# Optimization experiments

Measured on AMD Instinct MI355X. Metric: run time of the kernel, lower is better.

The kernel has to match this reference:

```python
import jax, jax.numpy as jnp
import numpy as np

BS, SEQ, E, H, NG, NH = 512, 32, 1024, 1024, 3, 2
MID = SEQ - NG + 1  # 30 (fusion_bidir is Linear(60, 30) -> 2*MID == 60)


def setup_inputs() -> dict:
    key = jax.random.key(0)
    ks = jax.random.split(key, 15)
    sE, sH, sNH = E ** -0.5, H ** -0.5, NH ** -0.5
    f32 = jnp.float32
    return {
        "x": jax.random.normal(ks[0], (BS, SEQ, E), f32),
        "h0": jax.random.normal(ks[1], (2, BS, H), f32),
        "Wz": jax.random.normal(ks[2], (2, H, E), f32) * sE,
        "Uz": jax.random.normal(ks[3], (2, H, H), f32) * sH,
        "Wr": jax.random.normal(ks[4], (2, H, E), f32) * sE,
        "Ur": jax.random.normal(ks[5], (2, H, H), f32) * sH,
        "Wh": jax.random.normal(ks[6], (2, H, E), f32) * sE,
        "Uh": jax.random.normal(ks[7], (2, H, H), f32) * sH,
        "Ua": jax.random.normal(ks[8], (2, NH, E), f32) * sE,      # Ua1: Linear(E,1) per head
        "Wa_w": jax.random.normal(ks[9], (2, NH, NG, H), f32) * sH, # Wa1: Linear(H,NG) per head
        "Wa_b": jax.random.normal(ks[10], (2, NH, NG), f32) * sH,
        "fh_w": jax.random.normal(ks[11], (2, NH), f32) * sNH,      # fusion_head: Linear(NH,1)
        "fh_b": jax.random.normal(ks[12], (2,), f32) * sNH,
        "fb_w": jax.random.normal(ks[13], (30, 60), f32) * (60 ** -0.5),
        "fb_b": jax.random.normal(ks[14], (30,), f32) * (60 ** -0.5),
    }


def _forward_dir(x, h0, Wz, Uz, Wr, Ur, Wh, Uh, Ua, Wa_w, Wa_b, fh_w, fh_b):
    # x: [bs, SEQ, E]; h0: [bs, H]; returns [bs, MID, E]
    idx = jnp.arange(MID)[:, None] + jnp.arange(NG)[None, :]   # [MID, NG]
    xw = x[:, idx, :]                                          # [bs, MID, NG, E] windows
    ua = jnp.einsum('bmge,he->bmgh', xw, Ua)                   # Ua1(x_) per head
    xs = xw.sum(2)                                             # [bs, MID, E] window sum
    # precompute input projections of GRU gates (big GEMMs, hoisted out of scan)
    pz = jnp.einsum('bme,de->bmd', xs, Wz)
    pr = jnp.einsum('bme,de->bmd', xs, Wr)
    ph = jnp.einsum('bme,de->bmd', xs, Wh)
    seqs = (ua.transpose(1, 0, 2, 3), xw.transpose(1, 0, 2, 3),
            pz.transpose(1, 0, 2), pr.transpose(1, 0, 2), ph.transpose(1, 0, 2))

    def step(ht, s):
        ua_t, xw_t, pz_t, pr_t, ph_t = s
        # attention scores: Ua1(x_) + Wa1(ht), fused over heads, tanh, softmax over window
        wa = jnp.einsum('bd,hgd->bgh', ht, Wa_w) + Wa_b.T[None]    # [bs, NG, NH]
        et = jnp.tanh(jnp.einsum('bgh,h->bg', ua_t + wa, fh_w) + fh_b)
        alpha = jax.nn.softmax(et, axis=1)                          # [bs, NG]
        out = jnp.einsum('bge,bg->be', xw_t, alpha)                 # weighted window sum
        # GRU gates on the (unweighted) window sum, as in the original
        zt = jax.nn.sigmoid(pz_t + ht @ Uz.T)
        rt = jax.nn.sigmoid(pr_t + ht @ Ur.T)
        hw = jnp.tanh(ph_t + (rt * ht) @ Uh.T)
        ht_new = (1.0 - zt) * ht + zt * hw
        return ht_new, out

    _, outs = jax.lax.scan(step, h0, seqs)       # outs: [MID, bs, E]
    return outs.transpose(1, 0, 2)


def reference(x, h0, Wz, Uz, Wr, Ur, Wh, Uh, Ua, Wa_w, Wa_b, fh_w, fh_b, fb_w, fb_b):
    X0 = _forward_dir(x, h0[0], Wz[0], Uz[0], Wr[0], Ur[0], Wh[0], Uh[0],
                      Ua[0], Wa_w[0], Wa_b[0], fh_w[0], fh_b[0])
    X1 = _forward_dir(x[:, ::-1, :], h0[1], Wz[1], Uz[1], Wr[1], Ur[1], Wh[1], Uh[1],
                      Ua[1], Wa_w[1], Wa_b[1], fh_w[1], fh_b[1])
    Xb = jnp.concatenate([X0, X1], axis=1).transpose(0, 2, 1)   # [bs, E, 2*MID]
    return (Xb @ fb_w.T + fb_b).transpose(0, 2, 1)              # [bs, 30, E]
```

## Files before the change

kernel.cpp:

```cpp
#include <hip/hip_runtime.h>
#include <hip/hip_bf16.h>
#include <math.h>

#define BSZ 512
#define SEQL 32
#define EDIM 1024
#define HDIM 1024
#define MIDL 30

typedef unsigned short u16;
typedef __attribute__((ext_vector_type(8))) short bf16x8_t;
typedef __attribute__((ext_vector_type(4))) float floatx4_t;

__device__ inline u16 f2bf(float v) {
    unsigned u = __float_as_uint(v);
    unsigned r = u + 0x7FFFu + ((u >> 16) & 1u);
    return (u16)(r >> 16);
}
__device__ inline float bf2f(u16 h) { return __uint_as_float(((unsigned)h) << 16); }
__device__ inline void split2(float v, u16& hi, u16& lo) {
    u16 h = f2bf(v);
    hi = h;
    lo = f2bf(v - bf2f(h));
}

#define SWZ(r, cb) (((r) << 7) + ((cb) ^ (((r) & 7) << 4)))

#define GLOAD16(g, l)                                                    \
    __builtin_amdgcn_global_load_lds(                                    \
        (const __attribute__((address_space(1))) void*)(g),              \
        (__attribute__((address_space(3))) void*)(l), 16, 0, 0)

__global__ __launch_bounds__(256) void convert_w(const float* __restrict__ src,
                                                 u16* __restrict__ hi,
                                                 u16* __restrict__ lo,
                                                 int writeLo) {
    size_t i = ((size_t)blockIdx.x * 256 + threadIdx.x) * 4;
    float4 v = *(const float4*)(src + i);
    u16 hx, lx, hy, ly, hz, lz, hw, lw;
    split2(v.x, hx, lx); split2(v.y, hy, ly);
    split2(v.z, hz, lz); split2(v.w, hw, lw);
    ushort4 hv; hv.x = hx; hv.y = hy; hv.z = hz; hv.w = hw;
    *(ushort4*)(hi + i) = hv;
    if (writeLo) {
        ushort4 lv; lv.x = lx; lv.y = ly; lv.z = lz; lv.w = lw;
        *(ushort4*)(lo + i) = lv;
    }
}

__global__ __launch_bounds__(256) void init_h(const float* __restrict__ h0,
                                              float* __restrict__ hbuf,
                                              u16* __restrict__ hhi,
                                              u16* __restrict__ hlo) {
    size_t i = ((size_t)blockIdx.x * 256 + threadIdx.x) * 4;
    float4 v = *(const float4*)(h0 + i);
    *(float4*)(hbuf + i) = v;
    u16 hx, lx, hy, ly, hz, lz, hw, lw;
    split2(v.x, hx, lx); split2(v.y, hy, ly);
    split2(v.z, hz, lz); split2(v.w, hw, lw);
    ushort4 hv; hv.x = hx; hv.y = hy; hv.z = hz; hv.w = hw;
    ushort4 lv; lv.x = lx; lv.y = ly; lv.z = lz; lv.w = lw;
    *(ushort4*)(hhi + i) = hv;
    *(ushort4*)(hlo + i) = lv;
}

__global__ __launch_bounds__(256) void xs_build(const float* __restrict__ x,
                                                u16* __restrict__ xshi,
                                                u16* __restrict__ xslo,
                                                int writeLo) {
    int idx = blockIdx.x * 256 + threadIdx.x;
    int vid = idx & 255;
    int bw = idx >> 8;
    int w = bw % 30, b = bw / 30;
    const float* s = x + ((size_t)b * SEQL + w) * EDIM + vid * 4;
    float4 a = *(const float4*)s;
    float4 c = *(const float4*)(s + EDIM);
    float4 e = *(const float4*)(s + 2 * EDIM);
    float4 v; v.x = a.x + c.x + e.x; v.y = a.y + c.y + e.y;
    v.z = a.z + c.z + e.z; v.w = a.w + c.w + e.w;
    size_t o = ((size_t)b * 30 + w) * EDIM + vid * 4;
    u16 hx, lx, hy, ly, hz, lz, hw, lw;
    split2(v.x, hx, lx); split2(v.y, hy, ly);
    split2(v.z, hz, lz); split2(v.w, hw, lw);
    ushort4 hv; hv.x = hx; hv.y = hy; hv.z = hz; hv.w = hw;
    *(ushort4*)(xshi + o) = hv;
    if (writeLo) {
        ushort4 lv; lv.x = lx; lv.y = ly; lv.z = lz; lv.w = lw;
        *(ushort4*)(xslo + o) = lv;
    }
}

__global__ __launch_bounds__(256) void ua2_kernel(const float* __restrict__ x,
                                                  const float* __restrict__ Ua,
                                                  float* __restrict__ ua2) {
    int bs = blockIdx.x;
    int b = bs >> 5, s = bs & 31;
    const float* xr = x + ((size_t)b * SEQL + s) * EDIM;
    int tid = threadIdx.x;
    float a[4] = {0.f, 0.f, 0.f, 0.f};
    for (int e = tid; e < EDIM; e += 256) {
        float xv = xr[e];
#pragma unroll
        for (int q = 0; q < 4; q++) a[q] += xv * Ua[q * EDIM + e];
    }
#pragma unroll
    for (int q = 0; q < 4; q++)
        for (int off = 32; off > 0; off >>= 1) a[q] += __shfl_down(a[q], off);
    __shared__ float sr[4][4];
    int wid = tid >> 6, lane = tid & 63;
    if (lane == 0) {
#pragma unroll
        for (int q = 0; q < 4; q++) sr[wid][q] = a[q];
    }
    __syncthreads();
    if (tid < 4) {
        float v = sr[0][tid] + sr[1][tid] + sr[2][tid] + sr[3][tid];
        int d = tid >> 1, h2 = tid & 1;
        ua2[(((size_t)d * BSZ + b) * SEQL + s) * 2 + h2] = v;
    }
}

template<int BM, int MODE, typename XT>
__global__ __launch_bounds__(256) void gemm_step(
    const u16* __restrict__ whi, const u16* __restrict__ wlo,
    const u16* __restrict__ ahi, const u16* __restrict__ alo,
    const u16* __restrict__ xshi, const u16* __restrict__ xslo,
    float* __restrict__ hbuf, float* __restrict__ zbuf,
    u16* __restrict__ ohi, u16* __restrict__ olo,
    const float* __restrict__ x, const float* __restrict__ ua2,
    const float* __restrict__ Wa_w, const float* __restrict__ Wa_b,
    const float* __restrict__ fh_w, const float* __restrict__ fh_b,
    XT* __restrict__ Xbuf,
    int m, int useXsLo, int useWLo) {

    constexpr int MF = BM / 32;
    constexpr int GX = 512 / BM;

    __shared__ __align__(16) u16 AsHi[BM * 64], AsLo[BM * 64];
    __shared__ __align__(16) u16 BsHi[64 * 64], BsLo[64 * 64];
    __shared__ float sred[4][6];

    const int d = blockIdx.z;
    const int tid = threadIdx.x;
    const int wid = tid >> 6, lane = tid & 63;

    if (MODE == 0 && blockIdx.y >= 32) {
        const int b = blockIdx.x * 64 + (blockIdx.y - 32);
        const float* hb = hbuf + ((size_t)d * BSZ + b) * HDIM;
        const float* Ww = Wa_w + (size_t)d * 6 * HDIM;
        float w6[6] = {0.f, 0.f, 0.f, 0.f, 0.f, 0.f};
        for (int j = tid; j < HDIM; j += 256) {
            float hv = hb[j];
#pragma unroll
            for (int q = 0; q < 6; q++) w6[q] += hv * Ww[q * HDIM + j];
        }
#pragma unroll
        for (int q = 0; q < 6; q++)
            for (int off = 32; off > 0; off >>= 1) w6[q] += __shfl_down(w6[q], off);
        if (lane == 0) {
#pragma unroll
            for (int q = 0; q < 6; q++) sred[wid][q] = w6[q];
        }
        __syncthreads();
        float s6[6];
#pragma unroll
        for (int q = 0; q < 6; q++)
            s6[q] = sred[0][q] + sred[1][q] + sred[2][q] + sred[3][q];

        int p0 = (d == 0) ? m : (31 - m);
        int p1 = (d == 0) ? (m + 1) : (30 - m);
        int p2 = (d == 0) ? (m + 2) : (29 - m);
        const float fw0 = fh_w[d * 2 + 0], fw1 = fh_w[d * 2 + 1], fbv = fh_b[d];
        float et[3];
        int pg[3] = {p0, p1, p2};
#pragma unroll
        for (int g = 0; g < 3; g++) {
            const float* u = ua2 + (((size_t)d * BSZ + b) * SEQL + pg[g]) * 2;
            float a0 = u[0] + s6[g] + Wa_b[d * 6 + g];
            float a1 = u[1] + s6[3 + g] + Wa_b[d * 6 + 3 + g];
            et[g] = tanhf(a0 * fw0 + a1 * fw1 + fbv);
        }
        float mx = fmaxf(et[0], fmaxf(et[1], et[2]));
        float e0 = expf(et[0] - mx), e1 = expf(et[1] - mx), e2 = expf(et[2] - mx);
        float inv = 1.f / (e0 + e1 + e2);
        float al0 = e0 * inv, al1 = e1 * inv, al2 = e2 * inv;

        const float* xb = x + (size_t)b * SEQL * EDIM;
        int e4 = tid * 4;
        float4 x0 = *(const float4*)(xb + (size_t)p0 * EDIM + e4);
        float4 x1 = *(const float4*)(xb + (size_t)p1 * EDIM + e4);
        float4 x2 = *(const float4*)(xb + (size_t)p2 * EDIM + e4);
        float4 v; v.x = al0 * x0.x + al1 * x1.x + al2 * x2.x;
        v.y = al0 * x0.y + al1 * x1.y + al2 * x2.y;
        v.z = al0 * x0.z + al1 * x1.z + al2 * x2.z;
        v.w = al0 * x0.w + al1 * x1.w + al2 * x2.w;
        XT* Xo = Xbuf + (((size_t)d * BSZ + b) * MIDL + m) * EDIM + e4;
        if constexpr (sizeof(XT) == 4) {
            *(float4*)Xo = v;
        } else {
            ushort4 uv; uv.x = f2bf(v.x); uv.y = f2bf(v.y);
            uv.z = f2bf(v.z); uv.w = f2bf(v.w);
            *(ushort4*)Xo = uv;
        }
        return;
    }

    const int lin = blockIdx.x + GX * blockIdx.y;
    const int work = (lin & 7) * 32 + (lin >> 3);
    const int b0 = (work & (GX - 1)) * BM;
    const int n0 = (work / GX) * 64;
    const int w = (d == 0) ? m : (29 - m);

    int rgate, nrow0, matU, matW;
    if (MODE == 0) {
        rgate = (n0 >= 1024) ? 1 : 0;
        nrow0 = n0 & 1023;
        matU = rgate ? 1 : 0;
        matW = rgate ? 4 : 3;
    } else {
        rgate = 0; nrow0 = n0; matU = 2; matW = 5;
    }

    floatx4_t acc[MF][2];
#pragma unroll
    for (int i = 0; i < MF; i++)
#pragma unroll
        for (int j = 0; j < 2; j++) acc[i][j] = (floatx4_t){0.f, 0.f, 0.f, 0.f};

    const int wm = wid >> 1, wn = wid & 1;
    const int rr = lane >> 3;
    const int swb = (((lane & 7) ^ rr) << 4);
    const int cA0 = wid, cA1 = wid + 4;
    const int cB0 = wid, cB1 = wid + 4;

    for (int half = 0; half < 2; half++) {
        const size_t wOff = (size_t)(half ? matW : matU) * 2097152 + (size_t)d * 1048576;
        const char* bH = (const char*)(whi + wOff);
        const char* bL = (const char*)(wlo + wOff);
        const int bLoOn = useWLo;
        int aLoOn;
        const char *pa0h, *pa0l, *pa1h = nullptr, *pa1l = nullptr;
        if (half == 0) {
            aLoOn = 1;
            size_t r0 = (size_t)(d * BSZ + b0 + cA0 * 8 + rr) * 2048;
            pa0h = (const char*)ahi + r0 + swb;
            pa0l = (const char*)alo + r0 + swb;
            if (BM == 64) {
                size_t r1 = (size_t)(d * BSZ + b0 + cA1 * 8 + rr) * 2048;
                pa1h = (const char*)ahi + r1 + swb;
                pa1l = (const char*)alo + r1 + swb;
            }
        } else {
            aLoOn = useXsLo;
            size_t r0 = ((size_t)(b0 + cA0 * 8 + rr) * 30 + w) * 2048;
            pa0h = (const char*)xshi + r0 + swb;
            pa0l = (const char*)xslo + r0 + swb;
            if (BM == 64) {
                size_t r1 = ((size_t)(b0 + cA1 * 8 + rr) * 30 + w) * 2048;
                pa1h = (const char*)xshi + r1 + swb;
                pa1l = (const char*)xslo + r1 + swb;
            }
        }
        size_t q0 = (size_t)(nrow0 + cB0 * 8 + rr) * 2048;
        size_t q1 = (size_t)(nrow0 + cB1 * 8 + rr) * 2048;
        const char* pb0h = bH + q0 + swb;
        const char* pb1h = bH + q1 + swb;
        const char* pb0l = bL + q0 + swb;
        const char* pb1l = bL + q1 + swb;

        for (int kk = 0; kk < 16; kk++) {
            const size_t ko = (size_t)kk * 128;
            __syncthreads();
            GLOAD16(pa0h + ko, (char*)AsHi + cA0 * 1024);
            if (BM == 64) GLOAD16(pa1h + ko, (char*)AsHi + cA1 * 1024);
            GLOAD16(pb0h + ko, (char*)BsHi + cB0 * 1024);
            GLOAD16(pb1h + ko, (char*)BsHi + cB1 * 1024);
            if (aLoOn) {
                GLOAD16(pa0l + ko, (char*)AsLo + cA0 * 1024);
                if (BM == 64) GLOAD16(pa1l + ko, (char*)AsLo + cA1 * 1024);
            }
            if (bLoOn) {
                GLOAD16(pb0l + ko, (char*)BsLo + cB0 * 1024);
                GLOAD16(pb1l + ko, (char*)BsLo + cB1 * 1024);
            }
            __syncthreads();

#pragma unroll
            for (int cc = 0; cc < 2; cc++) {
                const int cbyte = cc * 64 + ((lane >> 4) << 4);
                bf16x8_t ah_[MF], al_[MF], bh_[2], bl_[2];
#pragma unroll
                for (int mf = 0; mf < MF; mf++) {
                    int r = wm * (BM / 2) + mf * 16 + (lane & 15);
                    int ia = SWZ(r, cbyte) >> 1;
                    ah_[mf] = *(const bf16x8_t*)(AsHi + ia);
                    if (aLoOn) al_[mf] = *(const bf16x8_t*)(AsLo + ia);
                }
#pragma unroll
                for (int nf = 0; nf < 2; nf++) {
                    int r = wn * 32 + nf * 16 + (lane & 15);
                    int ib = SWZ(r, cbyte) >> 1;
                    bh_[nf] = *(const bf16x8_t*)(BsHi + ib);
                    if (bLoOn) bl_[nf] = *(const bf16x8_t*)(BsLo + ib);
                }
#pragma unroll
                for (int mf = 0; mf < MF; mf++)
#pragma unroll
                    for (int nf = 0; nf < 2; nf++) {
                        acc[mf][nf] = __builtin_amdgcn_mfma_f32_16x16x32_bf16(
                            ah_[mf], bh_[nf], acc[mf][nf], 0, 0, 0);
                        if (bLoOn)
                            acc[mf][nf] = __builtin_amdgcn_mfma_f32_16x16x32_bf16(
                                ah_[mf], bl_[nf], acc[mf][nf], 0, 0, 0);
                        if (aLoOn)
                            acc[mf][nf] = __builtin_amdgcn_mfma_f32_16x16x32_bf16(
                                al_[mf], bh_[nf], acc[mf][nf], 0, 0, 0);
                    }
            }
        }
    }

#pragma unroll
    for (int mf = 0; mf < MF; mf++)
#pragma unroll
        for (int nf = 0; nf < 2; nf++)
#pragma unroll
            for (int j = 0; j < 4; j++) {
                int bb = b0 + wm * (BM / 2) + mf * 16 + ((lane >> 4) << 2) + j;
                int nn = nrow0 + wn * 32 + nf * 16 + (lane & 15);
                size_t oi = ((size_t)d * BSZ + bb) * 1024 + nn;
                float v = acc[mf][nf][j];
                if (MODE == 0) {
                    float sg = 1.f / (1.f + expf(-v));
                    if (!rgate) {
                        zbuf[oi] = sg;
                    } else {
                        float rh = sg * hbuf[oi];
                        u16 h, l; split2(rh, h, l);
                        ohi[oi] = h; olo[oi] = l;
                    }
                } else {
                    float hw = tanhf(v);
                    float z = zbuf[oi], hv = hbuf[oi];
                    float hn = hv + z * (hw - hv);
                    hbuf[oi] = hn;
                    u16 h, l; split2(hn, h, l);
                    ohi[oi] = h; olo[oi] = l;
                }
            }
}

template<typename XT>
__global__ __launch_bounds__(256) void final_mix(const XT* __restrict__ Xbuf,
                                                 const float* __restrict__ fbw,
                                                 const float* __restrict__ fbb,
                                                 float* __restrict__ out) {
    __shared__ float sw[30][60];
    __shared__ float sb[30];
    const int tid = threadIdx.x;
    for (int i = tid; i < 1800; i += 256) sw[i / 60][i % 60] = fbw[i];
    if (tid < 30) sb[tid] = fbb[tid];
    __syncthreads();

    const int idx = blockIdx.x * 256 + tid;
    const int b = idx >> 10;
    const int e = idx & 1023;

    float accv[30];
#pragma unroll
    for (int mo = 0; mo < 30; mo++) accv[mo] = sb[mo];

    for (int dd = 0; dd < 2; dd++)
        for (int mm = 0; mm < 30; mm++) {
            float v;
            if constexpr (sizeof(XT) == 4)
                v = ((const float*)Xbuf)[(((size_t)dd * BSZ + b) * MIDL + mm) * EDIM + e];
            else
                v = bf2f(((const u16*)Xbuf)[(((size_t)dd * BSZ + b) * MIDL + mm) * EDIM + e]);
            int j = dd * 30 + mm;
#pragma unroll
            for (int mo = 0; mo < 30; mo++) accv[mo] += sw[mo][j] * v;
        }
    float* ob = out + (size_t)b * 30 * EDIM;
#pragma unroll
    for (int mo = 0; mo < 30; mo++) ob[(size_t)mo * EDIM + e] = accv[mo];
}

template<typename XT>
static void run_all(const float* x, const float* h0,
                    const float* Wz, const float* Uz, const float* Wr, const float* Ur,
                    const float* Wh, const float* Uh, const float* Ua,
                    const float* Wa_w, const float* Wa_b,
                    const float* fh_w, const float* fh_b,
                    const float* fb_w, const float* fb_b,
                    float* out,
                    float* hbuf, float* zbuf, float* ua2,
                    u16* whi, u16* wlo, u16* xshi, u16* xslo,
                    u16* hhi, u16* hlo, u16* rhhi, u16* rhlo,
                    XT* Xbuf, int useXsLo, int useWLo, hipStream_t stream) {
    convert_w<<<2048, 256, 0, stream>>>(Uz, whi + (size_t)0 * 2097152, wlo + (size_t)0 * 2097152, useWLo);
    convert_w<<<2048, 256, 0, stream>>>(Ur, whi + (size_t)1 * 2097152, wlo + (size_t)1 * 2097152, useWLo);
    convert_w<<<2048, 256, 0, stream>>>(Uh, whi + (size_t)2 * 2097152, wlo + (size_t)2 * 2097152, useWLo);
    convert_w<<<2048, 256, 0, stream>>>(Wz, whi + (size_t)3 * 2097152, wlo + (size_t)3 * 2097152, useWLo);
    convert_w<<<2048, 256, 0, stream>>>(Wr, whi + (size_t)4 * 2097152, wlo + (size_t)4 * 2097152, useWLo);
    convert_w<<<2048, 256, 0, stream>>>(Wh, whi + (size_t)5 * 2097152, wlo + (size_t)5 * 2097152, useWLo);
    init_h<<<1024, 256, 0, stream>>>(h0, hbuf, hhi, hlo);
    ua2_kernel<<<16384, 256, 0, stream>>>(x, Ua, ua2);
    xs_build<<<15360, 256, 0, stream>>>(x, xshi, xslo, useXsLo);

    for (int m = 0; m < MIDL; m++) {
        gemm_step<64, 0, XT><<<dim3(8, 32 + 64, 2), 256, 0, stream>>>(
            whi, wlo, hhi, hlo, xshi, xslo, hbuf, zbuf, rhhi, rhlo,
            x, ua2, Wa_w, Wa_b, fh_w, fh_b, Xbuf, m, useXsLo, useWLo);
        gemm_step<32, 1, XT><<<dim3(16, 16, 2), 256, 0, stream>>>(
            whi, wlo, rhhi, rhlo, xshi, xslo, hbuf, zbuf, hhi, hlo,
            x, ua2, Wa_w, Wa_b, fh_w, fh_b, Xbuf, m, useXsLo, useWLo);
    }
    final_mix<XT><<<2048, 256, 0, stream>>>(Xbuf, fb_w, fb_b, out);
}

extern "C" void kernel_launch(void* const* d_in, const int* in_sizes, int n_in,
                              void* d_out, int out_size, void* d_ws, size_t ws_size,
                              hipStream_t stream) {
    const float* x    = (const float*)d_in[0];
    const float* h0   = (const float*)d_in[1];
    const float* Wz   = (const float*)d_in[2];
    const float* Uz   = (const float*)d_in[3];
    const float* Wr   = (const float*)d_in[4];
    const float* Ur   = (const float*)d_in[5];
    const float* Wh   = (const float*)d_in[6];
    const float* Uh   = (const float*)d_in[7];
    const float* Ua   = (const float*)d_in[8];
    const float* Wa_w = (const float*)d_in[9];
    const float* Wa_b = (const float*)d_in[10];
    const float* fh_w = (const float*)d_in[11];
    const float* fh_b = (const float*)d_in[12];
    const float* fb_w = (const float*)d_in[13];
    const float* fb_b = (const float*)d_in[14];
    float* out = (float*)d_out;

    const size_t NEED1 = 256114688;
    const size_t NEED2 = 193200128;
    int useWLo = 1, useXsLo = 1;
    bool xf32 = (ws_size >= NEED1);
    bool tier3 = (!xf32 && ws_size < NEED2);
    if (tier3) { useWLo = 0; useXsLo = 0; }

    char* p = (char*)d_ws;
    auto take = [&](size_t n) { char* r = p; p += n; return r; };
    float* hbuf = (float*)take(4194304);
    float* zbuf = (float*)take(4194304);
    float* ua2  = (float*)take(262144);
    u16* whi  = (u16*)take(25165824);
    u16* wlo  = useWLo ? (u16*)take(25165824) : whi;
    u16* xshi = (u16*)take(31457280);
    u16* xslo = useXsLo ? (u16*)take(31457280) : xshi;
    u16* hhi  = (u16*)take(2097152);
    u16* hlo  = (u16*)take(2097152);
    u16* rhhi = (u16*)take(2097152);
    u16* rhlo = (u16*)take(2097152);

    if (xf32) {
        float* Xbuf = (float*)take(125829120);
        run_all<float>(x, h0, Wz, Uz, Wr, Ur, Wh, Uh, Ua, Wa_w, Wa_b, fh_w, fh_b,
                       fb_w, fb_b, out, hbuf, zbuf, ua2, whi, wlo, xshi, xslo,
                       hhi, hlo, rhhi, rhlo, Xbuf, useXsLo, useWLo, stream);
    } else {
        u16* Xbuf = (u16*)take(62914560);
        run_all<u16>(x, h0, Wz, Uz, Wr, Ur, Wh, Uh, Ua, Wa_w, Wa_b, fh_w, fh_b,
                     fb_w, fb_b, out, hbuf, zbuf, ua2, whi, wlo, xshi, xslo,
                     hhi, hlo, rhhi, rhlo, Xbuf, useXsLo, useWLo, stream);
    }
}
```

Baseline: 2.557 ms.

## Switch GEMMs to fp16 split-A with single weights, double-buffer LDS, vectorize final mix

Replaces the bf16 hi/lo three-MFMA scheme with fp16: weights and window sums are stored as a single fp16 value, and only the hidden-state operand keeps a hi/lo split. That leaves two MFMAs on the recurrent half of K and one on the input half. The K loop is merged into one 32-tile loop with double-buffered LDS, so the next tile's global-to-LDS load overlaps the current compute. It also fuses the six weight conversions into one launch and makes final_mix compute two output columns per thread. The cost is lower precision, since fp16 weights and inputs lose the lo correction and fp16 has a narrower range, plus more LDS per block.

```diff
diff --git a/kernel.cpp b/kernel.cpp
--- a/kernel.cpp
+++ b/kernel.cpp
@@ -9,7 +9,8 @@
 #define MIDL 30
 
 typedef unsigned short u16;
-typedef __attribute__((ext_vector_type(8))) short bf16x8_t;
+typedef _Float16 f16;
+typedef __attribute__((ext_vector_type(8))) _Float16 f16x8_t;
 typedef __attribute__((ext_vector_type(4))) float floatx4_t;
 
 __device__ inline u16 f2bf(float v) {
@@ -18,10 +19,15 @@
     return (u16)(r >> 16);
 }
 __device__ inline float bf2f(u16 h) { return __uint_as_float(((unsigned)h) << 16); }
-__device__ inline void split2(float v, u16& hi, u16& lo) {
-    u16 h = f2bf(v);
-    hi = h;
-    lo = f2bf(v - bf2f(h));
+
+__device__ inline u16 f2h(float v) {
+    f16 h = (f16)v; u16 r; __builtin_memcpy(&r, &h, 2); return r;
+}
+__device__ inline void splith(float v, u16& hi, u16& lo) {
+    f16 h = (f16)v;
+    f16 l = (f16)(v - (float)h);
+    __builtin_memcpy(&hi, &h, 2);
+    __builtin_memcpy(&lo, &l, 2);
 }
 
 #define SWZ(r, cb) (((r) << 7) + ((cb) ^ (((r) & 7) << 4)))
@@ -31,21 +37,18 @@
         (const __attribute__((address_space(1))) void*)(g),              \
         (__attribute__((address_space(3))) void*)(l), 16, 0, 0)
 
-__global__ __launch_bounds__(256) void convert_w(const float* __restrict__ src,
-                                                 u16* __restrict__ hi,
-                                                 u16* __restrict__ lo,
-                                                 int writeLo) {
-    size_t i = ((size_t)blockIdx.x * 256 + threadIdx.x) * 4;
+__global__ __launch_bounds__(256) void convert_w6(
+    const float* __restrict__ s0, const float* __restrict__ s1,
+    const float* __restrict__ s2, const float* __restrict__ s3,
+    const float* __restrict__ s4, const float* __restrict__ s5,
+    u16* __restrict__ whi) {
+    int mat = blockIdx.x >> 11;
+    const float* src = (mat == 0) ? s0 : (mat == 1) ? s1 : (mat == 2) ? s2
+                     : (mat == 3) ? s3 : (mat == 4) ? s4 : s5;
+    size_t i = ((size_t)(blockIdx.x & 2047) * 256 + threadIdx.x) * 4;
     float4 v = *(const float4*)(src + i);
-    u16 hx, lx, hy, ly, hz, lz, hw, lw;
-    split2(v.x, hx, lx); split2(v.y, hy, ly);
-    split2(v.z, hz, lz); split2(v.w, hw, lw);
-    ushort4 hv; hv.x = hx; hv.y = hy; hv.z = hz; hv.w = hw;
-    *(ushort4*)(hi + i) = hv;
-    if (writeLo) {
-        ushort4 lv; lv.x = lx; lv.y = ly; lv.z = lz; lv.w = lw;
-        *(ushort4*)(lo + i) = lv;
-    }
+    ushort4 hv; hv.x = f2h(v.x); hv.y = f2h(v.y); hv.z = f2h(v.z); hv.w = f2h(v.w);
+    *(ushort4*)(whi + (size_t)mat * 2097152 + i) = hv;
 }
 
 __global__ __launch_bounds__(256) void init_h(const float* __restrict__ h0,
@@ -56,8 +59,8 @@
     float4 v = *(const float4*)(h0 + i);
     *(float4*)(hbuf + i) = v;
     u16 hx, lx, hy, ly, hz, lz, hw, lw;
-    split2(v.x, hx, lx); split2(v.y, hy, ly);
-    split2(v.z, hz, lz); split2(v.w, hw, lw);
+    splith(v.x, hx, lx); splith(v.y, hy, ly);
+    splith(v.z, hz, lz); splith(v.w, hw, lw);
     ushort4 hv; hv.x = hx; hv.y = hy; hv.z = hz; hv.w = hw;
     ushort4 lv; lv.x = lx; lv.y = ly; lv.z = lz; lv.w = lw;
     *(ushort4*)(hhi + i) = hv;
@@ -65,9 +68,7 @@
 }
 
 __global__ __launch_bounds__(256) void xs_build(const float* __restrict__ x,
-                                                u16* __restrict__ xshi,
-                                                u16* __restrict__ xslo,
-                                                int writeLo) {
+                                                u16* __restrict__ xshi) {
     int idx = blockIdx.x * 256 + threadIdx.x;
     int vid = idx & 255;
     int bw = idx >> 8;
@@ -79,15 +80,8 @@
     float4 v; v.x = a.x + c.x + e.x; v.y = a.y + c.y + e.y;
     v.z = a.z + c.z + e.z; v.w = a.w + c.w + e.w;
     size_t o = ((size_t)b * 30 + w) * EDIM + vid * 4;
-    u16 hx, lx, hy, ly, hz, lz, hw, lw;
-    split2(v.x, hx, lx); split2(v.y, hy, ly);
-    split2(v.z, hz, lz); split2(v.w, hw, lw);
-    ushort4 hv; hv.x = hx; hv.y = hy; hv.z = hz; hv.w = hw;
+    ushort4 hv; hv.x = f2h(v.x); hv.y = f2h(v.y); hv.z = f2h(v.z); hv.w = f2h(v.w);
     *(ushort4*)(xshi + o) = hv;
-    if (writeLo) {
-        ushort4 lv; lv.x = lx; lv.y = ly; lv.z = lz; lv.w = lw;
-        *(ushort4*)(xslo + o) = lv;
-    }
 }
 
 __global__ __launch_bounds__(256) void ua2_kernel(const float* __restrict__ x,
@@ -122,22 +116,22 @@
 
 template<int BM, int MODE, typename XT>
 __global__ __launch_bounds__(256) void gemm_step(
-    const u16* __restrict__ whi, const u16* __restrict__ wlo,
+    const u16* __restrict__ whi,
     const u16* __restrict__ ahi, const u16* __restrict__ alo,
-    const u16* __restrict__ xshi, const u16* __restrict__ xslo,
+    const u16* __restrict__ xshi,
     float* __restrict__ hbuf, float* __restrict__ zbuf,
     u16* __restrict__ ohi, u16* __restrict__ olo,
     const float* __restrict__ x, const float* __restrict__ ua2,
     const float* __restrict__ Wa_w, const float* __restrict__ Wa_b,
     const float* __restrict__ fh_w, const float* __restrict__ fh_b,
-    XT* __restrict__ Xbuf,
-    int m, int useXsLo, int useWLo) {
+    XT* __restrict__ Xbuf, int m) {
 
     constexpr int MF = BM / 32;
     constexpr int GX = 512 / BM;
 
-    __shared__ __align__(16) u16 AsHi[BM * 64], AsLo[BM * 64];
-    __shared__ __align__(16) u16 BsHi[64 * 64], BsLo[64 * 64];
+    __shared__ __align__(16) u16 AsH[2][BM * 64];
+    __shared__ __align__(16) u16 AsL[2][BM * 64];
+    __shared__ __align__(16) u16 BsH[2][64 * 64];
     __shared__ float sred[4][6];
 
     const int d = blockIdx.z;
@@ -233,92 +227,87 @@
     const int cA0 = wid, cA1 = wid + 4;
     const int cB0 = wid, cB1 = wid + 4;
 
-    for (int half = 0; half < 2; half++) {
-        const size_t wOff = (size_t)(half ? matW : matU) * 2097152 + (size_t)d * 1048576;
-        const char* bH = (const char*)(whi + wOff);
-        const char* bL = (const char*)(wlo + wOff);
-        const int bLoOn = useWLo;
-        int aLoOn;
-        const char *pa0h, *pa0l, *pa1h = nullptr, *pa1l = nullptr;
-        if (half == 0) {
-            aLoOn = 1;
-            size_t r0 = (size_t)(d * BSZ + b0 + cA0 * 8 + rr) * 2048;
-            pa0h = (const char*)ahi + r0 + swb;
-            pa0l = (const char*)alo + r0 + swb;
-            if (BM == 64) {
-                size_t r1 = (size_t)(d * BSZ + b0 + cA1 * 8 + rr) * 2048;
-                pa1h = (const char*)ahi + r1 + swb;
-                pa1l = (const char*)alo + r1 + swb;
+    const u16* bU = whi + (size_t)matU * 2097152 + (size_t)d * 1048576;
+    const u16* bW = whi + (size_t)matW * 2097152 + (size_t)d * 1048576;
+    size_t ar0 = (size_t)(d * BSZ + b0 + cA0 * 8 + rr) * 2048;
+    size_t ar1 = (size_t)(d * BSZ + b0 + cA1 * 8 + rr) * 2048;
+    const char* pa0h = (const char*)ahi + ar0 + swb;
+    const char* pa0l = (const char*)alo + ar0 + swb;
+    const char* pa1h = (const char*)ahi + ar1 + swb;
+    const char* pa1l = (const char*)alo + ar1 + swb;
+    size_t xr0 = ((size_t)(b0 + cA0 * 8 + rr) * 30 + w) * 2048;
+    size_t xr1 = ((size_t)(b0 + cA1 * 8 + rr) * 30 + w) * 2048;
+    const char* px0 = (const char*)xshi + xr0 + swb;
+    const char* px1 = (const char*)xshi + xr1 + swb;
+    size_t q0 = (size_t)(nrow0 + cB0 * 8 + rr) * 2048;
+    size_t q1 = (size_t)(nrow0 + cB1 * 8 + rr) * 2048;
+    const char* pbU0 = (const char*)bU + q0 + swb;
+    const char* pbU1 = (const char*)bU + q1 + swb;
+    const char* pbW0 = (const char*)bW + q0 + swb;
+    const char* pbW1 = (const char*)bW + q1 + swb;
+
+    auto STAGE = [&](int kt, int pb) {
+        const size_t ko = (size_t)(kt & 15) * 128;
+        char* ah = (char*)AsH[pb];
+        char* al = (char*)AsL[pb];
+        char* bs = (char*)BsH[pb];
+        if (kt < 16) {
+            GLOAD16(pa0h + ko, ah + cA0 * 1024);
+            if constexpr (BM == 64) GLOAD16(pa1h + ko, ah + cA1 * 1024);
+            GLOAD16(pa0l + ko, al + cA0 * 1024);
+            if constexpr (BM == 64) GLOAD16(pa1l + ko, al + cA1 * 1024);
+            GLOAD16(pbU0 + ko, bs + cB0 * 1024);
+            GLOAD16(pbU1 + ko, bs + cB1 * 1024);
+        } else {
+            GLOAD16(px0 + ko, ah + cA0 * 1024);
+            if constexpr (BM == 64) GLOAD16(px1 + ko, ah + cA1 * 1024);
+            GLOAD16(pbW0 + ko, bs + cB0 * 1024);
+            GLOAD16(pbW1 + ko, bs + cB1 * 1024);
+        }
+    };
+
+    auto COMPUTE = [&](int kt, int pb) {
+        const bool hasLo = (kt < 16);
+#pragma unroll
+        for (int cc = 0; cc < 2; cc++) {
+            const int cbyte = cc * 64 + ((lane >> 4) << 4);
+            f16x8_t ah_[MF], al_[MF], bh_[2];
+#pragma unroll
+            for (int mf = 0; mf < MF; mf++) {
+                int r = wm * (BM / 2) + mf * 16 + (lane & 15);
+                int ia = SWZ(r, cbyte) >> 1;
+                ah_[mf] = *(const f16x8_t*)(AsH[pb] + ia);
+                if (hasLo) al_[mf] = *(const f16x8_t*)(AsL[pb] + ia);
             }
-        } else {
-            aLoOn = useXsLo;
-            size_t r0 = ((size_t)(b0 + cA0 * 8 + rr) * 30 + w) * 2048;
-            pa0h = (const char*)xshi + r0 + swb;
-            pa0l = (const char*)xslo + r0 + swb;
-            if (BM == 64) {
-                size_t r1 = ((size_t)(b0 + cA1 * 8 + rr) * 30 + w) * 2048;
-                pa1h = (const char*)xshi + r1 + swb;
-                pa1l = (const char*)xslo + r1 + swb;
+#pragma unroll
+            for (int nf = 0; nf < 2; nf++) {
+                int r = wn * 32 + nf * 16 + (lane & 15);
+                int ib = SWZ(r, cbyte) >> 1;
+                bh_[nf] = *(const f16x8_t*)(BsH[pb] + ib);
             }
-        }
-        size_t q0 = (size_t)(nrow0 + cB0 * 8 + rr) * 2048;
-        size_t q1 = (size_t)(nrow0 + cB1 * 8 + rr) * 2048;
-        const char* pb0h = bH + q0 + swb;
-        const char* pb1h = bH + q1 + swb;
-        const char* pb0l = bL + q0 + swb;
-        const char* pb1l = bL + q1 + swb;
-
-        for (int kk = 0; kk < 16; kk++) {
-            const size_t ko = (size_t)kk * 128;
-            __syncthreads();
-            GLOAD16(pa0h + ko, (char*)AsHi + cA0 * 1024);
-            if (BM == 64) GLOAD16(pa1h + ko, (char*)AsHi + cA1 * 1024);
-            GLOAD16(pb0h + ko, (char*)BsHi + cB0 * 1024);
-            GLOAD16(pb1h + ko, (char*)BsHi + cB1 * 1024);
-            if (aLoOn) {
-                GLOAD16(pa0l + ko, (char*)AsLo + cA0 * 1024);
-                if (BM == 64) GLOAD16(pa1l + ko, (char*)AsLo + cA1 * 1024);
-            }
-            if (bLoOn) {
-                GLOAD16(pb0l + ko, (char*)BsLo + cB0 * 1024);
-                GLOAD16(pb1l + ko, (char*)BsLo + cB1 * 1024);
-            }
-            __syncthreads();
-
-#pragma unroll
-            for (int cc = 0; cc < 2; cc++) {
-                const int cbyte = cc * 64 + ((lane >> 4) << 4);
-                bf16x8_t ah_[MF], al_[MF], bh_[2], bl_[2];
-#pragma unroll
-                for (int mf = 0; mf < MF; mf++) {
-                    int r = wm * (BM / 2) + mf * 16 + (lane & 15);
-                    int ia = SWZ(r, cbyte) >> 1;
-                    ah_[mf] = *(const bf16x8_t*)(AsHi + ia);
-                    if (aLoOn) al_[mf] = *(const bf16x8_t*)(AsLo + ia);
+#pragma unroll
+            for (int mf = 0; mf < MF; mf++)
+#pragma unroll
+                for (int nf = 0; nf < 2; nf++) {
+                    acc[mf][nf] = __builtin_amdgcn_mfma_f32_16x16x32_f16(
+                        ah_[mf], bh_[nf], acc[mf][nf], 0, 0, 0);
+                    if (hasLo)
+                        acc[mf][nf] = __builtin_amdgcn_mfma_f32_16x16x32_f16(
+                            al_[mf], bh_[nf], acc[mf][nf], 0, 0, 0);
                 }
-#pragma unroll
-                for (int nf = 0; nf < 2; nf++) {
-                    int r = wn * 32 + nf * 16 + (lane & 15);
-                    int ib = SWZ(r, cbyte) >> 1;
-                    bh_[nf] = *(const bf16x8_t*)(BsHi + ib);
-                    if (bLoOn) bl_[nf] = *(const bf16x8_t*)(BsLo + ib);
-                }
-#pragma unroll
-                for (int mf = 0; mf < MF; mf++)
-#pragma unroll
-                    for (int nf = 0; nf < 2; nf++) {
-                        acc[mf][nf] = __builtin_amdgcn_mfma_f32_16x16x32_bf16(
-                            ah_[mf], bh_[nf], acc[mf][nf], 0, 0, 0);
-                        if (bLoOn)
-                            acc[mf][nf] = __builtin_amdgcn_mfma_f32_16x16x32_bf16(
-                                ah_[mf], bl_[nf], acc[mf][nf], 0, 0, 0);
-                        if (aLoOn)
-                            acc[mf][nf] = __builtin_amdgcn_mfma_f32_16x16x32_bf16(
-                                al_[mf], bh_[nf], acc[mf][nf], 0, 0, 0);
-                    }
-            }
-        }
-    }
+        }
+    };
+
+    STAGE(0, 0);
+    __syncthreads();
+    int cur = 0;
+    for (int kt = 0; kt < 31; kt++) {
+        STAGE(kt + 1, cur ^ 1);
+        COMPUTE(kt, cur);
+        __syncthreads();
+        cur ^= 1;
+    }
+    COMPUTE(31, cur);
 
 #pragma unroll
     for (int mf = 0; mf < MF; mf++)
@@ -336,7 +325,7 @@
                         zbuf[oi] = sg;
                     } else {
                         float rh = sg * hbuf[oi];
-                        u16 h, l; split2(rh, h, l);
+                        u16 h, l; splith(rh, h, l);
                         ohi[oi] = h; olo[oi] = l;
                     }
                 } else {
@@ -344,7 +333,7 @@
                     float z = zbuf[oi], hv = hbuf[oi];
                     float hn = hv + z * (hw - hv);
                     hbuf[oi] = hn;
-                    u16 h, l; split2(hn, h, l);
+                    u16 h, l; splith(hn, h, l);
                     ohi[oi] = h; olo[oi] = l;
                 }
             }
@@ -355,35 +344,46 @@
                                                  const float* __restrict__ fbw,
                                                  const float* __restrict__ fbb,
                                                  float* __restrict__ out) {
-    __shared__ float sw[30][60];
+    __shared__ float sw[60][30];
     __shared__ float sb[30];
     const int tid = threadIdx.x;
-    for (int i = tid; i < 1800; i += 256) sw[i / 60][i % 60] = fbw[i];
+    for (int i = tid; i < 1800; i += 256) {
+        int mo = i / 60, j = i % 60;
+        sw[j][mo] = fbw[i];
+    }
     if (tid < 30) sb[tid] = fbb[tid];
     __syncthreads();
 
     const int idx = blockIdx.x * 256 + tid;
-    const int b = idx >> 10;
-    const int e = idx & 1023;
-
-    float accv[30];
-#pragma unroll
-    for (int mo = 0; mo < 30; mo++) accv[mo] = sb[mo];
+    const int b = idx >> 9;
+    const int e2 = (idx & 511) * 2;
+
+    float2 acc[30];
+#pragma unroll
+    for (int mo = 0; mo < 30; mo++) { acc[mo].x = sb[mo]; acc[mo].y = sb[mo]; }
 
     for (int dd = 0; dd < 2; dd++)
+#pragma unroll 2
         for (int mm = 0; mm < 30; mm++) {
-            float v;
-            if constexpr (sizeof(XT) == 4)
-                v = ((const float*)Xbuf)[(((size_t)dd * BSZ + b) * MIDL + mm) * EDIM + e];
-            else
-                v = bf2f(((const u16*)Xbuf)[(((size_t)dd * BSZ + b) * MIDL + mm) * EDIM + e]);
+            float2 v;
+            if constexpr (sizeof(XT) == 4) {
+                v = *(const float2*)((const float*)Xbuf +
+                    (((size_t)dd * BSZ + b) * MIDL + mm) * EDIM + e2);
+            } else {
+                const u16* s = (const u16*)Xbuf +
+                    (((size_t)dd * BSZ + b) * MIDL + mm) * EDIM + e2;
+                v.x = bf2f(s[0]); v.y = bf2f(s[1]);
+            }
             int j = dd * 30 + mm;
 #pragma unroll
-            for (int mo = 0; mo < 30; mo++) accv[mo] += sw[mo][j] * v;
-        }
-    float* ob = out + (size_t)b * 30 * EDIM;
-#pragma unroll
-    for (int mo = 0; mo < 30; mo++) ob[(size_t)mo * EDIM + e] = accv[mo];
+            for (int mo = 0; mo < 30; mo++) {
+                acc[mo].x += sw[j][mo] * v.x;
+                acc[mo].y += sw[j][mo] * v.y;
+            }
+        }
+    float* ob = out + (size_t)b * 30 * EDIM + e2;
+#pragma unroll
+    for (int mo = 0; mo < 30; mo++) *(float2*)(ob + (size_t)mo * EDIM) = acc[mo];
 }
 
 template<typename XT>
@@ -395,28 +395,23 @@
                     const float* fb_w, const float* fb_b,
                     float* out,
                     float* hbuf, float* zbuf, float* ua2,
-                    u16* whi, u16* wlo, u16* xshi, u16* xslo,
+                    u16* whi, u16* xshi,
                     u16* hhi, u16* hlo, u16* rhhi, u16* rhlo,
-                    XT* Xbuf, int useXsLo, int useWLo, hipStream_t stream) {
-    convert_w<<<2048, 256, 0, stream>>>(Uz, whi + (size_t)0 * 2097152, wlo + (size_t)0 * 2097152, useWLo);
-    convert_w<<<2048, 256, 0, stream>>>(Ur, whi + (size_t)1 * 2097152, wlo + (size_t)1 * 2097152, useWLo);
-    convert_w<<<2048, 256, 0, stream>>>(Uh, whi + (size_t)2 * 2097152, wlo + (size_t)2 * 2097152, useWLo);
-    convert_w<<<2048, 256, 0, stream>>>(Wz, whi + (size_t)3 * 2097152, wlo + (size_t)3 * 2097152, useWLo);
-    convert_w<<<2048, 256, 0, stream>>>(Wr, whi + (size_t)4 * 2097152, wlo + (size_t)4 * 2097152, useWLo);
-    convert_w<<<2048, 256, 0, stream>>>(Wh, whi + (size_t)5 * 2097152, wlo + (size_t)5 * 2097152, useWLo);
+                    XT* Xbuf, hipStream_t stream) {
+    convert_w6<<<12288, 256, 0, stream>>>(Uz, Ur, Uh, Wz, Wr, Wh, whi);
     init_h<<<1024, 256, 0, stream>>>(h0, hbuf, hhi, hlo);
     ua2_kernel<<<16384, 256, 0, stream>>>(x, Ua, ua2);
-    xs_build<<<15360, 256, 0, stream>>>(x, xshi, xslo, useXsLo);
+    xs_build<<<15360, 256, 0, stream>>>(x, xshi);
 
     for (int m = 0; m < MIDL; m++) {
         gemm_step<64, 0, XT><<<dim3(8, 32 + 64, 2), 256, 0, stream>>>(
-            whi, wlo, hhi, hlo, xshi, xslo, hbuf, zbuf, rhhi, rhlo,
-            x, ua2, Wa_w, Wa_b, fh_w, fh_b, Xbuf, m, useXsLo, useWLo);
+            whi, hhi, hlo, xshi, hbuf, zbuf, rhhi, rhlo,
+            x, ua2, Wa_w, Wa_b, fh_w, fh_b, Xbuf, m);
         gemm_step<32, 1, XT><<<dim3(16, 16, 2), 256, 0, stream>>>(
-            whi, wlo, rhhi, rhlo, xshi, xslo, hbuf, zbuf, hhi, hlo,
-            x, ua2, Wa_w, Wa_b, fh_w, fh_b, Xbuf, m, useXsLo, useWLo);
-    }
-    final_mix<XT><<<2048, 256, 0, stream>>>(Xbuf, fb_w, fb_b, out);
+            whi, rhhi, rhlo, xshi, hbuf, zbuf, hhi, hlo,
+            x, ua2, Wa_w, Wa_b, fh_w, fh_b, Xbuf, m);
+    }
+    final_mix<XT><<<1024, 256, 0, stream>>>(Xbuf, fb_w, fb_b, out);
 }
 
 extern "C" void kernel_launch(void* const* d_in, const int* in_sizes, int n_in,
@@ -439,12 +434,8 @@
     const float* fb_b = (const float*)d_in[14];
     float* out = (float*)d_out;
 
-    const size_t NEED1 = 256114688;
-    const size_t NEED2 = 193200128;
-    int useWLo = 1, useXsLo = 1;
+    const size_t NEED1 = 199491584;
     bool xf32 = (ws_size >= NEED1);
-    bool tier3 = (!xf32 && ws_size < NEED2);
-    if (tier3) { useWLo = 0; useXsLo = 0; }
 
     char* p = (char*)d_ws;
     auto take = [&](size_t n) { char* r = p; p += n; return r; };
@@ -452,9 +443,7 @@
     float* zbuf = (float*)take(4194304);
     float* ua2  = (float*)take(262144);
     u16* whi  = (u16*)take(25165824);
-    u16* wlo  = useWLo ? (u16*)take(25165824) : whi;
     u16* xshi = (u16*)take(31457280);
-    u16* xslo = useXsLo ? (u16*)take(31457280) : xshi;
     u16* hhi  = (u16*)take(2097152);
     u16* hlo  = (u16*)take(2097152);
     u16* rhhi = (u16*)take(2097152);
@@ -463,12 +452,12 @@
     if (xf32) {
         float* Xbuf = (float*)take(125829120);
         run_all<float>(x, h0, Wz, Uz, Wr, Ur, Wh, Uh, Ua, Wa_w, Wa_b, fh_w, fh_b,
-                       fb_w, fb_b, out, hbuf, zbuf, ua2, whi, wlo, xshi, xslo,
-                       hhi, hlo, rhhi, rhlo, Xbuf, useXsLo, useWLo, stream);
+                       fb_w, fb_b, out, hbuf, zbuf, ua2, whi, xshi,
+                       hhi, hlo, rhhi, rhlo, Xbuf, stream);
     } else {
         u16* Xbuf = (u16*)take(62914560);
         run_all<u16>(x, h0, Wz, Uz, Wr, Ur, Wh, Uh, Ua, Wa_w, Wa_b, fh_w, fh_b,
-                     fb_w, fb_b, out, hbuf, zbuf, ua2, whi, wlo, xshi, xslo,
-                     hhi, hlo, rhhi, rhlo, Xbuf, useXsLo, useWLo, stream);
-    }
-}
+                     fb_w, fb_b, out, hbuf, zbuf, ua2, whi, xshi,
+                     hhi, hlo, rhhi, rhlo, Xbuf, stream);
+    }
+}
```

Measured after the change: 2.477 ms. 1.03x faster.
